# Performance work log

Hardware: AMD Instinct MI355X
Metric: run time of the kernel (lower is better)

## Reference

```python
import jax, jax.numpy as jnp
import numpy as np

B, IN, OUT = 8192, 4096, 2048  # OUT must equal 32*64 per betta/gamma sizes


def setup_inputs() -> dict:
    key = jax.random.key(0)
    kx, kw = jax.random.split(key, 2)
    X = jax.random.normal(kx, (B, IN), dtype=jnp.float32)
    # xavier-uniform-like init for W
    limit = float(np.sqrt(6.0 / (IN + OUT)))
    W = jax.random.uniform(kw, (IN, OUT), minval=-limit, maxval=limit, dtype=jnp.float32)
    absmean = jnp.abs(W).mean(axis=0)
    alpha = jnp.abs(W).mean()          # scalar, >= 0
    betta = absmean[:32]               # (32,), >= 0
    gamma = absmean[32:96]             # (64,), >= 0
    return {"X": X, "W": W, "alpha": alpha, "betta": betta, "gamma": gamma}


def reference(X, W, alpha, betta, gamma):
    # module applies relu_ to alpha/betta/gamma data before the functional call
    alpha = jax.nn.relu(alpha)
    betta = jax.nn.relu(betta)
    gamma = jax.nn.relu(gamma)
    X_bin = jnp.sign(X)                # (B, IN)
    W_bin = jnp.sign(W)                # (IN, OUT)
    # scale[i*64+j] = alpha * betta[i] * gamma[j] -> (OUT,)
    scale = (alpha * jnp.outer(betta, gamma)).reshape(-1)
    return (X_bin @ W_bin) * scale     # (B, OUT)
```

## Files before the change

kernel.cpp:

```cpp
#include <hip/hip_runtime.h>


#define M_DIM 8192
#define K_DIM 4096
#define N_DIM 2048
#define NT2   (K_DIM / 128)
#define PANEL_A (128 * 256 * 16)
#define PANEL_B (128 * 128 * 16)
#define ATILE 16384
#define BTILE 8192

typedef int i32x4 __attribute__((ext_vector_type(4)));
typedef int i32x8 __attribute__((ext_vector_type(8)));
typedef float f32x16 __attribute__((ext_vector_type(16)));

__device__ __forceinline__ unsigned int nib4(float x) {
  unsigned int s = (__float_as_uint(x) >> 28) & 0x8u;
  return x == 0.0f ? 0u : (0x2u | s);
}

__device__ __forceinline__ unsigned int pack8(const float* f) {
  unsigned int p = 0;
#pragma unroll
  for (int j = 0; j < 8; ++j) p |= nib4(f[j]) << (4 * j);
  return p;
}

__device__ __forceinline__ void gload_lds16(const void* g, void* lds) {
  __builtin_amdgcn_global_load_lds(
      (const __attribute__((address_space(1))) unsigned int*)g,
      (__attribute__((address_space(3))) unsigned int*)lds, 16, 0, 0);
}

__device__ __forceinline__ i32x8 pad8(i32x4 v) {
  i32x8 r;
  r[0] = v[0]; r[1] = v[1]; r[2] = v[2]; r[3] = v[3];
  r[4] = 0; r[5] = 0; r[6] = 0; r[7] = 0;
  return r;
}

__global__ __launch_bounds__(256) void binX_kernel(
    const float* __restrict__ X, unsigned char* __restrict__ Xq) {
  __shared__ float tile[32][260];
  const int t = threadIdx.x;
  const int rg = blockIdx.x >> 4;
  const int kc = blockIdx.x & 15;
  const int lrow = t >> 6;
  const int col4 = (t & 63) * 4;
#pragma unroll
  for (int i = 0; i < 8; ++i)
    *(float4*)&tile[i * 4 + lrow][col4] =
        *(const float4*)&X[(size_t)(rg * 32 + i * 4 + lrow) * K_DIM + kc * 256 + col4];
  __syncthreads();
  const int s = t >> 5;
  const int r = t & 31;
  float f[32];
#pragma unroll
  for (int q = 0; q < 8; ++q)
    *(float4*)&f[q * 4] = *(const float4*)&tile[r][s * 32 + q * 4];
  uint4 gq;
  gq.x = pack8(f + 0);  gq.y = pack8(f + 8);
  gq.z = pack8(f + 16); gq.w = pack8(f + 24);
  const int row = rg * 32 + r;
  const int kslot = kc * 8 + s;
  unsigned char* dst = Xq + (size_t)(row >> 8) * PANEL_A +
                       ((size_t)kslot * 256 + (row & 255)) * 16;
  *(uint4*)dst = gq;
}

__global__ __launch_bounds__(256) void binW_kernel(
    const float* __restrict__ W, unsigned char* __restrict__ Wq) {
  __shared__ float tile[32][260];
  const int t = threadIdx.x;
  const int q = blockIdx.x >> 7;
  const int kt = (blockIdx.x >> 3) & 15;
  const int s = blockIdx.x & 7;
#pragma unroll
  for (int i = 0; i < 8; ++i) {
    int row = i * 4 + (t >> 6);
    int col4 = (t & 63) * 4;
    *(float4*)&tile[row][col4] =
        *(const float4*)&W[(size_t)(kt * 256 + s * 32 + row) * N_DIM + q * 256 + col4];
  }
  __syncthreads();
  float f[32];
#pragma unroll
  for (int k = 0; k < 32; ++k) f[k] = tile[k][t];
  uint4 gq;
  gq.x = pack8(f + 0);  gq.y = pack8(f + 8);
  gq.z = pack8(f + 16); gq.w = pack8(f + 24);
  const int n = q * 256 + t;
  const int kslot = kt * 8 + s;
  unsigned char* dst = Wq + (size_t)(n >> 7) * PANEL_B +
                       ((size_t)kslot * 128 + (n & 127)) * 16;
  *(uint4*)dst = gq;
}

__device__ __forceinline__ void stage_tiles(const unsigned char* __restrict__ Asrc,
                                            const unsigned char* __restrict__ Bsrc,
                                            unsigned char* ldsA, int t) {
#pragma unroll
  for (int p = 0; p < 4; ++p) {
    int c = p * 256 + t;
    gload_lds16(Asrc + c * 16, ldsA + c * 16);
  }
#pragma unroll
  for (int p = 0; p < 2; ++p) {
    int c = p * 256 + t;
    gload_lds16(Bsrc + c * 16, ldsA + 16384 + c * 16);
  }
}

__device__ __forceinline__ void load_frags(i32x4* a4, i32x4* b4,
                                           const unsigned char* pA,
                                           const unsigned char* pB,
                                           int g, int wr, int wc, int l31) {
#pragma unroll
  for (int fm = 0; fm < 4; ++fm)
    a4[fm] = *(const i32x4*)&pA[(g * 256 + wr * 128 + fm * 32 + l31) * 16];
#pragma unroll
  for (int fn = 0; fn < 2; ++fn)
    b4[fn] = *(const i32x4*)&pB[(g * 128 + wc * 64 + fn * 32 + l31) * 16];
}

__global__ __launch_bounds__(256, 2) void gemm_fp4_kernel(
    const unsigned char* __restrict__ Aq,
    const unsigned char* __restrict__ Bq,
    const float* __restrict__ alpha,
    const float* __restrict__ betta,
    const float* __restrict__ gamma,
    float* __restrict__ C) {
  __shared__ __align__(16) unsigned char smem[49152];

  const int t = threadIdx.x;
  const int lane = t & 63;
  const int l31 = lane & 31;
  const int lhi = lane >> 5;
  const int w = t >> 6;
  const int wr = w >> 1;
  const int wc = w & 1;

  const int bid = blockIdx.x;
  const int j = bid >> 3;
  const int bm = (bid & 7) * 4 + (j & 3);
  const int bn = j >> 2;
  const int row0 = bm * 256;
  const int col0 = bn * 128;

  const unsigned char* Abase = Aq + (size_t)bm * PANEL_A;
  const unsigned char* Bbase = Bq + (size_t)bn * PANEL_B;

  f32x16 acc[4][2];
#pragma unroll
  for (int fm = 0; fm < 4; ++fm)
#pragma unroll
    for (int fn = 0; fn < 2; ++fn)
#pragma unroll
      for (int r = 0; r < 16; ++r) acc[fm][fn][r] = 0.f;

  stage_tiles(Abase, Bbase, &smem[0], t);
  asm volatile("s_waitcnt vmcnt(0)" ::: "memory");
  __builtin_amdgcn_s_barrier();

  i32x4 a4[2][4], b4[2][2];
  load_frags(a4[0], b4[0], &smem[0], &smem[16384], lhi, wr, wc, l31);

  for (int kt = 0; kt < NT2; ++kt) {
    const int cur = kt & 1;
    const unsigned char* pA = &smem[cur * 24576];
    const unsigned char* pB = pA + 16384;

    asm volatile("s_waitcnt lgkmcnt(0)" ::: "memory");
    __builtin_amdgcn_sched_barrier(0);
    if (kt + 1 < NT2)
      stage_tiles(Abase + (kt + 1) * ATILE, Bbase + (kt + 1) * BTILE,
                  &smem[(cur ^ 1) * 24576], t);
    load_frags(a4[1], b4[1], pA, pB, 2 + lhi, wr, wc, l31);
    __builtin_amdgcn_sched_barrier(0);
    __builtin_amdgcn_s_setprio(1);
#pragma unroll
    for (int fm = 0; fm < 4; ++fm) {
      i32x8 av = pad8(a4[0][fm]);
#pragma unroll
      for (int fn = 0; fn < 2; ++fn)
        acc[fm][fn] = __builtin_amdgcn_mfma_scale_f32_32x32x64_f8f6f4(
            av, pad8(b4[0][fn]), acc[fm][fn], 4, 4,
            0, 0x7F7F7F7F, 0, 0x7F7F7F7F);
    }
    __builtin_amdgcn_s_setprio(0);

    asm volatile("s_waitcnt lgkmcnt(0)" ::: "memory");
    __builtin_amdgcn_sched_barrier(0);
    __builtin_amdgcn_s_setprio(1);
#pragma unroll
    for (int fm = 0; fm < 4; ++fm) {
      i32x8 av = pad8(a4[1][fm]);
#pragma unroll
      for (int fn = 0; fn < 2; ++fn)
        acc[fm][fn] = __builtin_amdgcn_mfma_scale_f32_32x32x64_f8f6f4(
            av, pad8(b4[1][fn]), acc[fm][fn], 4, 4,
            0, 0x7F7F7F7F, 0, 0x7F7F7F7F);
    }
    __builtin_amdgcn_s_setprio(0);

    asm volatile("s_waitcnt vmcnt(0)" ::: "memory");
    __builtin_amdgcn_s_barrier();
    if (kt + 1 < NT2) {
      const unsigned char* nA = &smem[((kt + 1) & 1) * 24576];
      load_frags(a4[0], b4[0], nA, nA + 16384, lhi, wr, wc, l31);
    }
  }

  const float ra = fmaxf(alpha[0], 0.0f);
#pragma unroll
  for (int fn = 0; fn < 2; ++fn) {
    const int col = col0 + wc * 64 + fn * 32 + l31;
    const float sc = ra * fmaxf(betta[col >> 6], 0.0f) * fmaxf(gamma[col & 63], 0.0f);
#pragma unroll
    for (int fm = 0; fm < 4; ++fm) {
      const int rbase = row0 + wr * 128 + fm * 32 + 4 * lhi;
#pragma unroll
      for (int r = 0; r < 16; ++r) {
        const int row = rbase + (r & 3) + 8 * (r >> 2);
        C[(size_t)row * N_DIM + col] = acc[fm][fn][r] * sc;
      }
    }
  }
}

extern "C" void kernel_launch(void* const* d_in, const int* in_sizes, int n_in,
                              void* d_out, int out_size, void* d_ws, size_t ws_size,
                              hipStream_t stream) {
  const float* X = (const float*)d_in[0];
  const float* W = (const float*)d_in[1];
  const float* alpha = (const float*)d_in[2];
  const float* betta = (const float*)d_in[3];
  const float* gamma = (const float*)d_in[4];
  float* out = (float*)d_out;

  unsigned char* Xq = (unsigned char*)d_ws;
  unsigned char* Wq = Xq + (size_t)(M_DIM / 256) * PANEL_A;

  binW_kernel<<<1024, 256, 0, stream>>>(W, Wq);
  binX_kernel<<<4096, 256, 0, stream>>>(X, Xq);
  gemm_fp4_kernel<<<(M_DIM / 256) * (N_DIM / 128), 256, 0, stream>>>(
      Xq, Wq, alpha, betta, gamma, out);
}
```

Measured before the change: 74.55 us.

## Shrink GEMM tile to 128x128 and raise occupancy, drop fragment prefetch

```diff
diff --git a/kernel.cpp b/kernel.cpp
--- a/kernel.cpp
+++ b/kernel.cpp
@@ -4,11 +4,9 @@
 #define M_DIM 8192
 #define K_DIM 4096
 #define N_DIM 2048
-#define NT2   (K_DIM / 128)
-#define PANEL_A (128 * 256 * 16)
-#define PANEL_B (128 * 128 * 16)
-#define ATILE 16384
-#define BTILE 8192
+#define NTK   (K_DIM / 128)
+#define PANEL (128 * 128 * 16)
+#define KTILE 8192
 
 typedef int i32x4 __attribute__((ext_vector_type(4)));
 typedef int i32x8 __attribute__((ext_vector_type(8)));
@@ -30,13 +28,6 @@
   __builtin_amdgcn_global_load_lds(
       (const __attribute__((address_space(1))) unsigned int*)g,
       (__attribute__((address_space(3))) unsigned int*)lds, 16, 0, 0);
-}
-
-__device__ __forceinline__ i32x8 pad8(i32x4 v) {
-  i32x8 r;
-  r[0] = v[0]; r[1] = v[1]; r[2] = v[2]; r[3] = v[3];
-  r[4] = 0; r[5] = 0; r[6] = 0; r[7] = 0;
-  return r;
 }
 
 __global__ __launch_bounds__(256) void binX_kernel(
@@ -63,8 +54,8 @@
   gq.z = pack8(f + 16); gq.w = pack8(f + 24);
   const int row = rg * 32 + r;
   const int kslot = kc * 8 + s;
-  unsigned char* dst = Xq + (size_t)(row >> 8) * PANEL_A +
-                       ((size_t)kslot * 256 + (row & 255)) * 16;
+  unsigned char* dst = Xq + (size_t)(row >> 7) * PANEL +
+                       ((size_t)kslot * 128 + (row & 127)) * 16;
   *(uint4*)dst = gq;
 }
 
@@ -91,46 +82,30 @@
   gq.z = pack8(f + 16); gq.w = pack8(f + 24);
   const int n = q * 256 + t;
   const int kslot = kt * 8 + s;
-  unsigned char* dst = Wq + (size_t)(n >> 7) * PANEL_B +
+  unsigned char* dst = Wq + (size_t)(n >> 7) * PANEL +
                        ((size_t)kslot * 128 + (n & 127)) * 16;
   *(uint4*)dst = gq;
 }
 
 __device__ __forceinline__ void stage_tiles(const unsigned char* __restrict__ Asrc,
                                             const unsigned char* __restrict__ Bsrc,
-                                            unsigned char* ldsA, int t) {
-#pragma unroll
-  for (int p = 0; p < 4; ++p) {
-    int c = p * 256 + t;
-    gload_lds16(Asrc + c * 16, ldsA + c * 16);
-  }
+                                            unsigned char* lds, int t) {
 #pragma unroll
   for (int p = 0; p < 2; ++p) {
     int c = p * 256 + t;
-    gload_lds16(Bsrc + c * 16, ldsA + 16384 + c * 16);
-  }
-}
-
-__device__ __forceinline__ void load_frags(i32x4* a4, i32x4* b4,
-                                           const unsigned char* pA,
-                                           const unsigned char* pB,
-                                           int g, int wr, int wc, int l31) {
-#pragma unroll
-  for (int fm = 0; fm < 4; ++fm)
-    a4[fm] = *(const i32x4*)&pA[(g * 256 + wr * 128 + fm * 32 + l31) * 16];
-#pragma unroll
-  for (int fn = 0; fn < 2; ++fn)
-    b4[fn] = *(const i32x4*)&pB[(g * 128 + wc * 64 + fn * 32 + l31) * 16];
-}
-
-__global__ __launch_bounds__(256, 2) void gemm_fp4_kernel(
+    gload_lds16(Asrc + c * 16, lds + c * 16);
+    gload_lds16(Bsrc + c * 16, lds + 8192 + c * 16);
+  }
+}
+
+__global__ __launch_bounds__(256, 4) void gemm_fp4_kernel(
     const unsigned char* __restrict__ Aq,
     const unsigned char* __restrict__ Bq,
     const float* __restrict__ alpha,
     const float* __restrict__ betta,
     const float* __restrict__ gamma,
     float* __restrict__ C) {
-  __shared__ __align__(16) unsigned char smem[49152];
+  __shared__ __align__(16) unsigned char smem[32768];
 
   const int t = threadIdx.x;
   const int lane = t & 63;
@@ -142,73 +117,61 @@
 
   const int bid = blockIdx.x;
   const int j = bid >> 3;
-  const int bm = (bid & 7) * 4 + (j & 3);
-  const int bn = j >> 2;
-  const int row0 = bm * 256;
+  const int bn = j & 15;
+  const int bm = (bid & 7) * 8 + (j >> 4);
+  const int row0 = bm * 128;
   const int col0 = bn * 128;
 
-  const unsigned char* Abase = Aq + (size_t)bm * PANEL_A;
-  const unsigned char* Bbase = Bq + (size_t)bn * PANEL_B;
-
-  f32x16 acc[4][2];
-#pragma unroll
-  for (int fm = 0; fm < 4; ++fm)
+  const unsigned char* Abase = Aq + (size_t)bm * PANEL;
+  const unsigned char* Bbase = Bq + (size_t)bn * PANEL;
+
+  f32x16 acc[2][2];
+#pragma unroll
+  for (int fm = 0; fm < 2; ++fm)
 #pragma unroll
     for (int fn = 0; fn < 2; ++fn)
 #pragma unroll
       for (int r = 0; r < 16; ++r) acc[fm][fn][r] = 0.f;
+
+  i32x8 a8[2], b8[2];
+#pragma unroll
+  for (int i = 0; i < 2; ++i)
+#pragma unroll
+    for (int e = 0; e < 8; ++e) { a8[i][e] = 0; b8[i][e] = 0; }
 
   stage_tiles(Abase, Bbase, &smem[0], t);
   asm volatile("s_waitcnt vmcnt(0)" ::: "memory");
   __builtin_amdgcn_s_barrier();
 
-  i32x4 a4[2][4], b4[2][2];
-  load_frags(a4[0], b4[0], &smem[0], &smem[16384], lhi, wr, wc, l31);
-
-  for (int kt = 0; kt < NT2; ++kt) {
+  for (int kt = 0; kt < NTK; ++kt) {
     const int cur = kt & 1;
-    const unsigned char* pA = &smem[cur * 24576];
-    const unsigned char* pB = pA + 16384;
-
-    asm volatile("s_waitcnt lgkmcnt(0)" ::: "memory");
-    __builtin_amdgcn_sched_barrier(0);
-    if (kt + 1 < NT2)
-      stage_tiles(Abase + (kt + 1) * ATILE, Bbase + (kt + 1) * BTILE,
-                  &smem[(cur ^ 1) * 24576], t);
-    load_frags(a4[1], b4[1], pA, pB, 2 + lhi, wr, wc, l31);
-    __builtin_amdgcn_sched_barrier(0);
-    __builtin_amdgcn_s_setprio(1);
-#pragma unroll
-    for (int fm = 0; fm < 4; ++fm) {
-      i32x8 av = pad8(a4[0][fm]);
+    const unsigned char* pA = &smem[cur * 16384];
+    const unsigned char* pB = pA + 8192;
+
+    if (kt + 1 < NTK)
+      stage_tiles(Abase + (kt + 1) * KTILE, Bbase + (kt + 1) * KTILE,
+                  &smem[(cur ^ 1) * 16384], t);
+
+#pragma unroll
+    for (int kk = 0; kk < 2; ++kk) {
+      const int g = kk * 2 + lhi;
+#pragma unroll
+      for (int fm = 0; fm < 2; ++fm)
+        *(i32x4*)&a8[fm] = *(const i32x4*)&pA[(g * 128 + wr * 64 + fm * 32 + l31) * 16];
 #pragma unroll
       for (int fn = 0; fn < 2; ++fn)
-        acc[fm][fn] = __builtin_amdgcn_mfma_scale_f32_32x32x64_f8f6f4(
-            av, pad8(b4[0][fn]), acc[fm][fn], 4, 4,
-            0, 0x7F7F7F7F, 0, 0x7F7F7F7F);
+        *(i32x4*)&b8[fn] = *(const i32x4*)&pB[(g * 128 + wc * 64 + fn * 32 + l31) * 16];
+#pragma unroll
+      for (int fm = 0; fm < 2; ++fm)
+#pragma unroll
+        for (int fn = 0; fn < 2; ++fn)
+          acc[fm][fn] = __builtin_amdgcn_mfma_scale_f32_32x32x64_f8f6f4(
+              a8[fm], b8[fn], acc[fm][fn], 4, 4,
+              0, 0x7F7F7F7F, 0, 0x7F7F7F7F);
     }
-    __builtin_amdgcn_s_setprio(0);
-
-    asm volatile("s_waitcnt lgkmcnt(0)" ::: "memory");
-    __builtin_amdgcn_sched_barrier(0);
-    __builtin_amdgcn_s_setprio(1);
-#pragma unroll
-    for (int fm = 0; fm < 4; ++fm) {
-      i32x8 av = pad8(a4[1][fm]);
-#pragma unroll
-      for (int fn = 0; fn < 2; ++fn)
-        acc[fm][fn] = __builtin_amdgcn_mfma_scale_f32_32x32x64_f8f6f4(
-            av, pad8(b4[1][fn]), acc[fm][fn], 4, 4,
-            0, 0x7F7F7F7F, 0, 0x7F7F7F7F);
-    }
-    __builtin_amdgcn_s_setprio(0);
 
     asm volatile("s_waitcnt vmcnt(0)" ::: "memory");
     __builtin_amdgcn_s_barrier();
-    if (kt + 1 < NT2) {
-      const unsigned char* nA = &smem[((kt + 1) & 1) * 24576];
-      load_frags(a4[0], b4[0], nA, nA + 16384, lhi, wr, wc, l31);
-    }
   }
 
   const float ra = fmaxf(alpha[0], 0.0f);
@@ -217,8 +180,8 @@
     const int col = col0 + wc * 64 + fn * 32 + l31;
     const float sc = ra * fmaxf(betta[col >> 6], 0.0f) * fmaxf(gamma[col & 63], 0.0f);
 #pragma unroll
-    for (int fm = 0; fm < 4; ++fm) {
-      const int rbase = row0 + wr * 128 + fm * 32 + 4 * lhi;
+    for (int fm = 0; fm < 2; ++fm) {
+      const int rbase = row0 + wr * 64 + fm * 32 + 4 * lhi;
 #pragma unroll
       for (int r = 0; r < 16; ++r) {
         const int row = rbase + (r & 3) + 8 * (r >> 2);
@@ -239,10 +202,10 @@
   float* out = (float*)d_out;
 
   unsigned char* Xq = (unsigned char*)d_ws;
-  unsigned char* Wq = Xq + (size_t)(M_DIM / 256) * PANEL_A;
+  unsigned char* Wq = Xq + (size_t)(M_DIM / 128) * PANEL;
 
   binW_kernel<<<1024, 256, 0, stream>>>(W, Wq);
   binX_kernel<<<4096, 256, 0, stream>>>(X, Xq);
-  gemm_fp4_kernel<<<(M_DIM / 256) * (N_DIM / 128), 256, 0, stream>>>(
+  gemm_fp4_kernel<<<(M_DIM / 128) * (N_DIM / 128), 256, 0, stream>>>(
       Xq, Wq, alpha, betta, gamma, out);
 }
```

Measured after the change: 75.75 us. About the same (+1.6%).
